# Optimization experiments

Hardware: AMD Instinct MI355X
Metric: run time of the kernel (lower is better)

Reference implementation:

```python
import jax, jax.numpy as jnp
import numpy as np

B, IN_SHAPE, EXP_SHAPE, HID, NB_CLASSES = 64, 10000, 53, 1500, 2048


def setup_inputs() -> dict:
    key = jax.random.key(0)
    ks = jax.random.split(key, 8)
    gos = jax.random.uniform(ks[0], (B, IN_SHAPE), dtype=jnp.float32)
    exp_x = jax.random.uniform(ks[1], (B, EXP_SHAPE), dtype=jnp.float32)
    # FlatModel params (torch Linear: y = x @ W.T + b; store pre-transposed)
    W1 = jax.random.normal(ks[2], (IN_SHAPE, HID), dtype=jnp.float32) * (1.0 / np.sqrt(IN_SHAPE))
    b1 = jnp.zeros((HID,), dtype=jnp.float32)
    W2 = jax.random.normal(ks[3], (HID + EXP_SHAPE, NB_CLASSES), dtype=jnp.float32) * (1.0 / np.sqrt(HID + EXP_SHAPE))
    b2 = jnp.zeros((NB_CLASSES,), dtype=jnp.float32)
    # HPO adjacency (non-trainable buffer in the original; values in [0,1))
    hpo_matrix = jax.random.uniform(ks[4], (NB_CLASSES, NB_CLASSES), dtype=jnp.float32)
    return {"gos": gos, "exp_x": exp_x, "W1": W1, "b1": b1, "W2": W2, "b2": b2, "hpo_matrix": hpo_matrix}


def reference(gos, exp_x, W1, b1, W2, b2, hpo_matrix):
    # FlatModel (eval mode: dropout is identity). torch F.gelu default = exact erf gelu.
    h = jax.nn.gelu(gos @ W1 + b1, approximate=False)          # (B, HID)
    x = jnp.concatenate([h, exp_x], axis=1)                     # (B, HID+EXP)
    flat = jax.nn.sigmoid(x @ W2 + b2)                          # (B, C)
    # HPOLayer + permute + MaxPool1d(C): out[b,j] = max_i flat[b,j] * M[i,j]
    out = jnp.max(flat[:, None, :] * hpo_matrix[None, :, :], axis=1)  # (B, C)
    return out
```

## Files before the change

### kernel.cpp

```cpp
#include <hip/hip_runtime.h>
#include <math.h>

#define B64 64
#define IN_SH 10000
#define GOSLD 10240
#define EXP_SH 53
#define HID 1500
#define NPAD1 1536
#define NBC 2048
#define K2 1553
#define XLD 1664
#define KS1 40
#define KCH1 256
#define KST1 8
#define KS2 13
#define KCH2 128
#define KST2 4
#define CMCH 32

using short8  = __attribute__((ext_vector_type(8))) short;
using floatx4 = __attribute__((ext_vector_type(4))) float;
using uintx4  = __attribute__((ext_vector_type(4))) unsigned int;

__device__ __forceinline__ unsigned short f2bf(float f) {
    unsigned u = __float_as_uint(f);
    u += 0x7fffu + ((u >> 16) & 1u);
    return (unsigned short)(u >> 16);
}

__global__ __launch_bounds__(256) void pre_k(const float* __restrict__ g,
                                             unsigned short* __restrict__ gb,
                                             const float* __restrict__ M,
                                             float* __restrict__ cm) {
    int bi = blockIdx.x;
    if (bi < 320) {
        int idx = bi * 256 + threadIdx.x;
        int b = idx / (GOSLD / 8);
        int k = (idx % (GOSLD / 8)) * 8;
        unsigned int o[4] = {0u, 0u, 0u, 0u};
        if (k < IN_SH) {
            const float* p = g + (size_t)b * IN_SH + k;
            #pragma unroll
            for (int i = 0; i < 4; i++) {
                float lo = p[2 * i], hi = p[2 * i + 1];
                o[i] = (unsigned)f2bf(lo) | ((unsigned)f2bf(hi) << 16);
            }
        }
        uintx4 v; v.x = o[0]; v.y = o[1]; v.z = o[2]; v.w = o[3];
        *(uintx4*)(gb + (size_t)b * GOSLD + k) = v;
    } else {
        int ci = bi - 320;
        int j  = (ci & 7) * 256 + threadIdx.x;
        int i0 = (ci >> 3) * 64;
        float m = 0.0f;
        #pragma unroll 16
        for (int i = i0; i < i0 + 64; i++)
            m = fmaxf(m, M[(size_t)i * NBC + j]);
        cm[(ci >> 3) * NBC + j] = m;
    }
}

__device__ __forceinline__ void load_step(
    const float* __restrict__ W, const unsigned short* __restrict__ brow0,
    int kb, int K, int ldw, int ldb, int cW, bool nok,
    float wv[8], uintx4 bv[4])
{
    #pragma unroll
    for (int j = 0; j < 8; j++) {
        int k = kb + j;
        wv[j] = (nok && k < K) ? W[(size_t)k * ldw + cW] : 0.f;
    }
    #pragma unroll
    for (int s = 0; s < 4; s++)
        bv[s] = *(const uintx4*)(brow0 + (size_t)s * 16 * ldb + kb);
}

template<int KSTEPS>
__global__ __launch_bounds__(256) void mfma_gemm(
    const float* __restrict__ W, const unsigned short* __restrict__ Bm,
    float* __restrict__ part, int N, int Npad, int K, int ldw, int ldb,
    int kchunk)
{
    int tid  = threadIdx.x;
    int w    = tid >> 6;
    int lane = tid & 63;
    int q    = lane >> 4;
    int l15  = lane & 15;
    int n0   = blockIdx.x * 64;
    int k0   = blockIdx.y * kchunk;
    int cW   = n0 + 16 * w + l15;
    bool nok = cW < N;
    int qk   = q * 8;

    floatx4 acc[4];
    #pragma unroll
    for (int s = 0; s < 4; s++) acc[s] = (floatx4){0.f, 0.f, 0.f, 0.f};

    const unsigned short* brow0 = Bm + (size_t)l15 * ldb;

    float  wv[2][8];
    uintx4 bv[2][4];
    load_step(W, brow0, k0 + qk, K, ldw, ldb, cW, nok, wv[0], bv[0]);
    if (KSTEPS > 1)
        load_step(W, brow0, k0 + 32 + qk, K, ldw, ldb, cW, nok, wv[1], bv[1]);

    #pragma unroll
    for (int st = 0; st < KSTEPS; st++) {
        const int p = st & 1;
        float  wt[8];
        uintx4 bt[4];
        if (st + 2 < KSTEPS)
            load_step(W, brow0, k0 + (st + 2) * 32 + qk, K, ldw, ldb, cW, nok, wt, bt);

        short8 af;
        #pragma unroll
        for (int j = 0; j < 8; j++) af[j] = (short)f2bf(wv[p][j]);
        #pragma unroll
        for (int s = 0; s < 4; s++) {
            short8 bf8 = __builtin_bit_cast(short8, bv[p][s]);
            acc[s] = __builtin_amdgcn_mfma_f32_16x16x32_bf16(af, bf8, acc[s], 0, 0, 0);
        }

        if (st + 2 < KSTEPS) {
            #pragma unroll
            for (int j = 0; j < 8; j++) wv[p][j] = wt[j];
            #pragma unroll
            for (int s = 0; s < 4; s++) bv[p][s] = bt[s];
        }
    }

    size_t base = (size_t)blockIdx.y * Npad * 64;
    int nrow = n0 + 16 * w + q * 4;
    #pragma unroll
    for (int s = 0; s < 4; s++) {
        #pragma unroll
        for (int r = 0; r < 4; r++)
            part[base + (size_t)(nrow + r) * 64 + s * 16 + l15] = acc[s][r];
    }
}

__global__ __launch_bounds__(256) void combine1(
    const float* __restrict__ part, const float* __restrict__ b1,
    const float* __restrict__ expx, unsigned short* __restrict__ X)
{
    int idx = blockIdx.x * 256 + threadIdx.x;
    int b = idx & 63;
    int n = idx >> 6;
    float v = 0.f;
    if (n < HID) {
        float s = 0.f;
        #pragma unroll
        for (int c = 0; c < KS1; c++)
            s += part[((size_t)c * NPAD1 + n) * 64 + b];
        s += b1[n];
        v = 0.5f * s * (1.0f + erff(s * 0.70710678118654752f));
    } else if (n < HID + EXP_SH) {
        v = expx[b * EXP_SH + (n - HID)];
    }
    X[(size_t)b * XLD + n] = f2bf(v);
}

__global__ __launch_bounds__(256) void final_k(
    const float* __restrict__ part2, const float* __restrict__ b2,
    const float* __restrict__ cm, float* __restrict__ out)
{
    int idx = blockIdx.x * 256 + threadIdx.x;
    int b = idx & 63;
    int j = idx >> 6;
    float s = 0.f;
    #pragma unroll
    for (int c = 0; c < KS2; c++)
        s += part2[((size_t)c * NBC + j) * 64 + b];
    s += b2[j];
    float sig = 1.0f / (1.0f + expf(-s));
    float m = 0.f;
    #pragma unroll
    for (int c = 0; c < CMCH; c++) m = fmaxf(m, cm[c * NBC + j]);
    out[(size_t)b * NBC + j] = sig * m;
}

extern "C" void kernel_launch(void* const* d_in, const int* in_sizes, int n_in,
                              void* d_out, int out_size, void* d_ws, size_t ws_size,
                              hipStream_t stream) {
    const float* gos  = (const float*)d_in[0];
    const float* expx = (const float*)d_in[1];
    const float* W1   = (const float*)d_in[2];
    const float* b1   = (const float*)d_in[3];
    const float* W2   = (const float*)d_in[4];
    const float* b2   = (const float*)d_in[5];
    const float* hpo  = (const float*)d_in[6];
    float* out = (float*)d_out;

    char* ws = (char*)d_ws;
    unsigned short* gosB = (unsigned short*)ws;
    float* part1 = (float*)(ws + 1310720);
    unsigned short* X = (unsigned short*)(ws + 1310720 + 15728640);
    float* part2 = (float*)(ws + 1310720 + 15728640 + 212992);
    float* cm    = (float*)(ws + 1310720 + 15728640 + 212992 + 6815744);

    pre_k<<<576, 256, 0, stream>>>(gos, gosB, hpo, cm);

    mfma_gemm<KST1><<<dim3(NPAD1 / 64, KS1), 256, 0, stream>>>(
        W1, gosB, part1, HID, NPAD1, IN_SH, HID, GOSLD, KCH1);

    combine1<<<(B64 * XLD) / 256, 256, 0, stream>>>(part1, b1, expx, X);

    mfma_gemm<KST2><<<dim3(NBC / 64, KS2), 256, 0, stream>>>(
        W2, X, part2, NBC, NBC, K2, NBC, XLD, KCH2);

    final_k<<<(B64 * NBC) / 256, 256, 0, stream>>>(part2, b2, cm, out);
}
```

Measured before the change: 170.6 us.

## Replace split-K partial buffers with atomicAdd into zeroed accumulators

Both split-K GEMMs now accumulate their partial tiles straight into one compact accumulator with float atomicAdd, where before each wrote its own partial slab. The accumulators are zeroed by extra blocks in the preprocessing kernel. The combine and final kernels then read a single value instead of summing 40 or 13 partials. This removes roughly 22 MB of partial-sum writes and reads, at the cost of atomic contention and a summation order that is no longer deterministic.

```diff
diff --git a/kernel.cpp b/kernel.cpp
--- a/kernel.cpp
+++ b/kernel.cpp
@@ -17,6 +17,7 @@
 #define KCH2 128
 #define KST2 4
 #define CMCH 32
+#define ACCF (NPAD1 * B64 + NBC * B64)
 
 using short8  = __attribute__((ext_vector_type(8))) short;
 using floatx4 = __attribute__((ext_vector_type(4))) float;
@@ -31,7 +32,8 @@
 __global__ __launch_bounds__(256) void pre_k(const float* __restrict__ g,
                                              unsigned short* __restrict__ gb,
                                              const float* __restrict__ M,
-                                             float* __restrict__ cm) {
+                                             float* __restrict__ cm,
+                                             float* __restrict__ accz) {
     int bi = blockIdx.x;
     if (bi < 320) {
         int idx = bi * 256 + threadIdx.x;
@@ -48,7 +50,7 @@
         }
         uintx4 v; v.x = o[0]; v.y = o[1]; v.z = o[2]; v.w = o[3];
         *(uintx4*)(gb + (size_t)b * GOSLD + k) = v;
-    } else {
+    } else if (bi < 576) {
         int ci = bi - 320;
         int j  = (ci & 7) * 256 + threadIdx.x;
         int i0 = (ci >> 3) * 64;
@@ -57,6 +59,12 @@
         for (int i = i0; i < i0 + 64; i++)
             m = fmaxf(m, M[(size_t)i * NBC + j]);
         cm[(ci >> 3) * NBC + j] = m;
+    } else {
+        int t = (bi - 576) * 256 + threadIdx.x;
+        floatx4 z = (floatx4){0.f, 0.f, 0.f, 0.f};
+        #pragma unroll
+        for (int i = 0; i < 28; i++)
+            *(floatx4*)(accz + (size_t)(i * 2048 + t) * 4) = z;
     }
 }
 
@@ -78,8 +86,7 @@
 template<int KSTEPS>
 __global__ __launch_bounds__(256) void mfma_gemm(
     const float* __restrict__ W, const unsigned short* __restrict__ Bm,
-    float* __restrict__ part, int N, int Npad, int K, int ldw, int ldb,
-    int kchunk)
+    float* __restrict__ accbuf, int N, int K, int ldw, int ldb, int kchunk)
 {
     int tid  = threadIdx.x;
     int w    = tid >> 6;
@@ -129,18 +136,17 @@
         }
     }
 
-    size_t base = (size_t)blockIdx.y * Npad * 64;
     int nrow = n0 + 16 * w + q * 4;
     #pragma unroll
     for (int s = 0; s < 4; s++) {
         #pragma unroll
         for (int r = 0; r < 4; r++)
-            part[base + (size_t)(nrow + r) * 64 + s * 16 + l15] = acc[s][r];
+            atomicAdd(&accbuf[(size_t)(nrow + r) * 64 + s * 16 + l15], acc[s][r]);
     }
 }
 
 __global__ __launch_bounds__(256) void combine1(
-    const float* __restrict__ part, const float* __restrict__ b1,
+    const float* __restrict__ hpre, const float* __restrict__ b1,
     const float* __restrict__ expx, unsigned short* __restrict__ X)
 {
     int idx = blockIdx.x * 256 + threadIdx.x;
@@ -148,11 +154,7 @@
     int n = idx >> 6;
     float v = 0.f;
     if (n < HID) {
-        float s = 0.f;
-        #pragma unroll
-        for (int c = 0; c < KS1; c++)
-            s += part[((size_t)c * NPAD1 + n) * 64 + b];
-        s += b1[n];
+        float s = hpre[(size_t)n * 64 + b] + b1[n];
         v = 0.5f * s * (1.0f + erff(s * 0.70710678118654752f));
     } else if (n < HID + EXP_SH) {
         v = expx[b * EXP_SH + (n - HID)];
@@ -161,17 +163,13 @@
 }
 
 __global__ __launch_bounds__(256) void final_k(
-    const float* __restrict__ part2, const float* __restrict__ b2,
+    const float* __restrict__ logits, const float* __restrict__ b2,
     const float* __restrict__ cm, float* __restrict__ out)
 {
     int idx = blockIdx.x * 256 + threadIdx.x;
     int b = idx & 63;
     int j = idx >> 6;
-    float s = 0.f;
-    #pragma unroll
-    for (int c = 0; c < KS2; c++)
-        s += part2[((size_t)c * NBC + j) * 64 + b];
-    s += b2[j];
+    float s = logits[(size_t)j * 64 + b] + b2[j];
     float sig = 1.0f / (1.0f + expf(-s));
     float m = 0.f;
     #pragma unroll
@@ -193,20 +191,20 @@
 
     char* ws = (char*)d_ws;
     unsigned short* gosB = (unsigned short*)ws;
-    float* part1 = (float*)(ws + 1310720);
-    unsigned short* X = (unsigned short*)(ws + 1310720 + 15728640);
-    float* part2 = (float*)(ws + 1310720 + 15728640 + 212992);
-    float* cm    = (float*)(ws + 1310720 + 15728640 + 212992 + 6815744);
-
-    pre_k<<<576, 256, 0, stream>>>(gos, gosB, hpo, cm);
+    float* hpre   = (float*)(ws + 1310720);
+    float* logits = (float*)(ws + 1310720 + 393216);
+    unsigned short* X = (unsigned short*)(ws + 1310720 + 393216 + 524288);
+    float* cm = (float*)(ws + 1310720 + 393216 + 524288 + 212992);
+
+    pre_k<<<584, 256, 0, stream>>>(gos, gosB, hpo, cm, hpre);
 
     mfma_gemm<KST1><<<dim3(NPAD1 / 64, KS1), 256, 0, stream>>>(
-        W1, gosB, part1, HID, NPAD1, IN_SH, HID, GOSLD, KCH1);
-
-    combine1<<<(B64 * XLD) / 256, 256, 0, stream>>>(part1, b1, expx, X);
+        W1, gosB, hpre, HID, IN_SH, HID, GOSLD, KCH1);
+
+    combine1<<<(B64 * XLD) / 256, 256, 0, stream>>>(hpre, b1, expx, X);
 
     mfma_gemm<KST2><<<dim3(NBC / 64, KS2), 256, 0, stream>>>(
-        W2, X, part2, NBC, NBC, K2, NBC, XLD, KCH2);
-
-    final_k<<<(B64 * NBC) / 256, 256, 0, stream>>>(part2, b2, cm, out);
-}
+        W2, X, logits, NBC, K2, NBC, XLD, KCH2);
+
+    final_k<<<(B64 * NBC) / 256, 256, 0, stream>>>(logits, b2, cm, out);
+}
```

Result: no change. 167.6 us (-1.7%).
